# Optimization experiments

Measured on AMD Instinct MI355X. Metric: run time of the kernel, lower is better.

## Reference

```python
import jax, jax.numpy as jnp
import numpy as np

B, C, H, W = 8, 512, 32, 32


def setup_inputs() -> dict:
    key = jax.random.key(0)
    kx, kq, kk, k6 = jax.random.split(key, 4)
    std = 0.02
    return {
        "x": jax.random.normal(kx, (B, C, H, W), dtype=jnp.float32),
        "Wq": jax.random.normal(kq, (C, C), dtype=jnp.float32) * std,
        "bq": jnp.zeros((C,), dtype=jnp.float32),
        "Wk": jax.random.normal(kk, (C, C), dtype=jnp.float32) * std,
        "bk": jnp.zeros((C,), dtype=jnp.float32),
        "W6": jax.random.normal(k6, (C, C), dtype=jnp.float32) * std,
        "b6": jnp.zeros((C,), dtype=jnp.float32),
    }


def reference(x, Wq, bq, Wk, bk, W6, b6):
    b, c, h, w = x.shape
    hw = h * w
    scale = 1.0 / (c ** 0.5)
    # [B, HW, C] token-major view of the feature map
    xf = jnp.transpose(x.reshape(b, c, hw), (0, 2, 1))
    # 1x1 convs are per-pixel linear layers (weight layout: [C_out, C_in])
    q = xf @ Wq.T + bq                      # [B, HW, C]
    k = xf @ Wk.T + bk                      # [B, HW, C]
    # cross-batch attention scores: every pixel attends to every pixel of every image
    scores = q.reshape(b * hw, c) @ k.reshape(b * hw, c).T   # [B*HW, B*HW]
    s = scores.reshape(b * hw, b, hw)
    # per-query: max response within each image, then mean over images
    xw = jnp.max(s, axis=-1).mean(axis=-1)  # [B*HW]
    xw = xw.reshape(b, hw) * scale
    xw = jax.nn.softmax(xw, axis=-1).reshape(b, 1, h, w)
    x5 = x * xw                             # spatial gating
    # final 1x1 conv
    of = jnp.transpose(x5.reshape(b, c, hw), (0, 2, 1)) @ W6.T + b6
    return jnp.transpose(of, (0, 2, 1)).reshape(b, c, h, w)
```

## Files before the change

kernel.cpp:

```cpp
#include <hip/hip_runtime.h>


typedef __attribute__((ext_vector_type(8))) short bf16x8;
typedef __attribute__((ext_vector_type(4))) float f32x4;

__device__ __forceinline__ unsigned short f2bf(float f) {
  unsigned u = __builtin_bit_cast(unsigned, f);
  u += 0x7FFFu + ((u >> 16) & 1u);
  return (unsigned short)(u >> 16);
}

__device__ __forceinline__ void gload_lds16(const void* g, void* l) {
  __builtin_amdgcn_global_load_lds(
      (const __attribute__((address_space(1))) unsigned int*)g,
      (__attribute__((address_space(3))) unsigned int*)l, 16, 0, 0);
}

__global__ __launch_bounds__(256) void transpose_x(const float* __restrict__ x,
                                                   short* __restrict__ xt) {
  const int p0 = blockIdx.x * 64, c0 = blockIdx.y * 64, b = blockIdx.z;
  __shared__ float t[64][65];
  const int u = threadIdx.x;
  {
    const int p4 = u & 15, cr = u >> 4;
    for (int cc = 0; cc < 4; ++cc) {
      const int c = cc * 16 + cr;
      const float4 v = *(const float4*)&x[((size_t)(b * 512 + c0 + c)) * 1024 + p0 + p4 * 4];
      t[p4 * 4 + 0][c] = v.x;
      t[p4 * 4 + 1][c] = v.y;
      t[p4 * 4 + 2][c] = v.z;
      t[p4 * 4 + 3][c] = v.w;
    }
  }
  __syncthreads();
  {
    const int c4 = u & 15, pr = u >> 4;
    for (int pp = 0; pp < 4; ++pp) {
      const int p = pp * 16 + pr;
      ushort4 o;
      o.x = f2bf(t[p][c4 * 4 + 0]);
      o.y = f2bf(t[p][c4 * 4 + 1]);
      o.z = f2bf(t[p][c4 * 4 + 2]);
      o.w = f2bf(t[p][c4 * 4 + 3]);
      *(ushort4*)&xt[((size_t)(b * 1024 + p0 + p)) * 512 + c0 + c4 * 4] = o;
    }
  }
}

__global__ __launch_bounds__(256) void pack_w(const float* __restrict__ Wq,
                                              const float* __restrict__ Wk,
                                              const float* __restrict__ W6,
                                              short* __restrict__ wcat) {
  const int i = blockIdx.x * 256 + threadIdx.x;
  const int idx = i * 4;
  const float* src = (idx < 262144) ? Wq : (idx < 524288) ? Wk : W6;
  const float4 v = *(const float4*)&src[idx & 262143];
  ushort4 o;
  o.x = f2bf(v.x); o.y = f2bf(v.y); o.z = f2bf(v.z); o.w = f2bf(v.w);
  *(ushort4*)&wcat[idx] = o;
}

__global__ __launch_bounds__(256) void gemm_qkz(const short* __restrict__ xt,
                                                const short* __restrict__ wcat,
                                                const float* __restrict__ bq,
                                                const float* __restrict__ bk,
                                                short* __restrict__ qk,
                                                float* __restrict__ z) {
  __shared__ short lds_a[128 * 32];
  __shared__ short lds_b[128 * 32];
  const int tid = threadIdx.x;
  const int w = tid >> 6, lane = tid & 63;
  const int wr = w >> 1, wc = w & 1;
  const int quad = lane >> 4, lcol = lane & 15;
  const int srow = w * 16 + (lane >> 2);
  const int skoff = (lane & 3) * 8;
  const int m0 = blockIdx.x * 128;
  const int n0 = blockIdx.y * 128;

  f32x4 acc[4][4];
#pragma unroll
  for (int i = 0; i < 4; ++i)
#pragma unroll
    for (int j = 0; j < 4; ++j)
#pragma unroll
      for (int r = 0; r < 4; ++r) acc[i][j][r] = 0.f;

  const short* Abase = xt + (size_t)(m0 + srow) * 512 + skoff;
  const short* Bbase = wcat + (size_t)(n0 + srow) * 512 + skoff;
  short* la = lds_a + (w * 16) * 32;
  short* lb = lds_b + (w * 16) * 32;

  for (int kt = 0; kt < 16; ++kt) {
    const int kb = kt * 32;
    __syncthreads();
    gload_lds16(Abase + kb, la);
    gload_lds16(Abase + kb + (size_t)64 * 512, la + 64 * 32);
    gload_lds16(Bbase + kb, lb);
    gload_lds16(Bbase + kb + (size_t)64 * 512, lb + 64 * 32);
    __syncthreads();
    bf16x8 af[4], bf[4];
#pragma unroll
    for (int i = 0; i < 4; ++i)
      af[i] = *(const bf16x8*)&lds_a[(wr * 64 + i * 16 + lcol) * 32 + quad * 8];
#pragma unroll
    for (int j = 0; j < 4; ++j)
      bf[j] = *(const bf16x8*)&lds_b[(wc * 64 + j * 16 + lcol) * 32 + quad * 8];
#pragma unroll
    for (int i = 0; i < 4; ++i)
#pragma unroll
      for (int j = 0; j < 4; ++j)
        acc[i][j] = __builtin_amdgcn_mfma_f32_16x16x32_bf16(af[i], bf[j], acc[i][j], 0, 0, 0);
  }

  const int region = (int)blockIdx.y >> 2;
  if (region < 2) {
    const float* bias = region ? bk : bq;
#pragma unroll
    for (int i = 0; i < 4; ++i)
#pragma unroll
      for (int j = 0; j < 4; ++j) {
        const int row = m0 + wr * 64 + i * 16 + quad * 4;
        const int col = n0 + wc * 64 + j * 16 + lcol;
        const float bv = bias[col & 511];
#pragma unroll
        for (int r = 0; r < 4; ++r)
          qk[(size_t)(row + r) * 1024 + col] = (short)f2bf(acc[i][j][r] + bv);
      }
  } else {
#pragma unroll
    for (int i = 0; i < 4; ++i)
#pragma unroll
      for (int j = 0; j < 4; ++j) {
        const int row = m0 + wr * 64 + i * 16 + quad * 4;
        const int col = n0 - 1024 + wc * 64 + j * 16 + lcol;
#pragma unroll
        for (int r = 0; r < 4; ++r)
          z[(size_t)(row + r) * 512 + col] = acc[i][j][r];
      }
  }
}

__global__ __launch_bounds__(256) void gemm_scores(const short* __restrict__ qk,
                                                   float* __restrict__ wsmx) {
  __shared__ short lds_a[128 * 32];
  __shared__ short lds_b[128 * 32];
  __shared__ float partial[128][2];
  const int tid = threadIdx.x;
  const int w = tid >> 6, lane = tid & 63;
  const int wr = w >> 1, wc = w & 1;
  const int quad = lane >> 4, lcol = lane & 15;
  const int srow = w * 16 + (lane >> 2);
  const int skoff = (lane & 3) * 8;
  const int m0 = blockIdx.x * 128;
  const int n0 = blockIdx.y * 128;

  f32x4 acc[4][4];
#pragma unroll
  for (int i = 0; i < 4; ++i)
#pragma unroll
    for (int j = 0; j < 4; ++j)
#pragma unroll
      for (int r = 0; r < 4; ++r) acc[i][j][r] = 0.f;

  const short* Abase = qk + (size_t)(m0 + srow) * 1024 + skoff;
  const short* Bbase = qk + (size_t)(n0 + srow) * 1024 + 512 + skoff;
  short* la = lds_a + (w * 16) * 32;
  short* lb = lds_b + (w * 16) * 32;

  for (int kt = 0; kt < 16; ++kt) {
    const int kb = kt * 32;
    __syncthreads();
    gload_lds16(Abase + kb, la);
    gload_lds16(Abase + kb + (size_t)64 * 1024, la + 64 * 32);
    gload_lds16(Bbase + kb, lb);
    gload_lds16(Bbase + kb + (size_t)64 * 1024, lb + 64 * 32);
    __syncthreads();
    bf16x8 af[4], bf[4];
#pragma unroll
    for (int i = 0; i < 4; ++i)
      af[i] = *(const bf16x8*)&lds_a[(wr * 64 + i * 16 + lcol) * 32 + quad * 8];
#pragma unroll
    for (int j = 0; j < 4; ++j)
      bf[j] = *(const bf16x8*)&lds_b[(wc * 64 + j * 16 + lcol) * 32 + quad * 8];
#pragma unroll
    for (int i = 0; i < 4; ++i)
#pragma unroll
      for (int j = 0; j < 4; ++j)
        acc[i][j] = __builtin_amdgcn_mfma_f32_16x16x32_bf16(af[i], bf[j], acc[i][j], 0, 0, 0);
  }

#pragma unroll
  for (int i = 0; i < 4; ++i) {
#pragma unroll
    for (int r = 0; r < 4; ++r) {
      float v = fmaxf(fmaxf(acc[i][0][r], acc[i][1][r]),
                      fmaxf(acc[i][2][r], acc[i][3][r]));
#pragma unroll
      for (int off = 1; off < 16; off <<= 1) v = fmaxf(v, __shfl_xor(v, off));
      if (lcol == 0) partial[wr * 64 + i * 16 + quad * 4 + r][wc] = v;
    }
  }
  __syncthreads();
  if (tid < 128)
    wsmx[(size_t)blockIdx.y * 8192 + m0 + tid] = fmaxf(partial[tid][0], partial[tid][1]);
}

__global__ __launch_bounds__(1024) void softmax_xw(const float* __restrict__ wsmx,
                                                   float* __restrict__ xw) {
  const int b = blockIdx.x, p = threadIdx.x;
  const int m = b * 1024 + p;
  float s = 0.f;
#pragma unroll
  for (int img = 0; img < 8; ++img) {
    float mx = -1e30f;
#pragma unroll
    for (int t = 0; t < 8; ++t) mx = fmaxf(mx, wsmx[(size_t)(img * 8 + t) * 8192 + m]);
    s += mx;
  }
  const float logit = s * 0.005524271728019903f;
  __shared__ float red[16];
  float v = logit;
#pragma unroll
  for (int off = 32; off >= 1; off >>= 1) v = fmaxf(v, __shfl_xor(v, off));
  if ((p & 63) == 0) red[p >> 6] = v;
  __syncthreads();
  float bmax = red[0];
#pragma unroll
  for (int t = 1; t < 16; ++t) bmax = fmaxf(bmax, red[t]);
  const float e = expf(logit - bmax);
  float sv = e;
#pragma unroll
  for (int off = 32; off >= 1; off >>= 1) sv += __shfl_xor(sv, off);
  __syncthreads();
  if ((p & 63) == 0) red[p >> 6] = sv;
  __syncthreads();
  float bsum = 0.f;
#pragma unroll
  for (int t = 0; t < 16; ++t) bsum += red[t];
  xw[m] = e / bsum;
}

__global__ __launch_bounds__(256) void epilogue_out(const float* __restrict__ z,
                                                    const float* __restrict__ xw,
                                                    const float* __restrict__ b6,
                                                    float* __restrict__ out) {
  const int p0 = blockIdx.x * 64, c0 = blockIdx.y * 64, b = blockIdx.z;
  __shared__ float t[64][65];
  const int u = threadIdx.x;
  {
    const int c4 = u & 15, pr = u >> 4;
    for (int pp = 0; pp < 4; ++pp) {
      const int p = pp * 16 + pr;
      const float4 v = *(const float4*)&z[((size_t)(b * 1024 + p0 + p)) * 512 + c0 + c4 * 4];
      t[c4 * 4 + 0][p] = v.x;
      t[c4 * 4 + 1][p] = v.y;
      t[c4 * 4 + 2][p] = v.z;
      t[c4 * 4 + 3][p] = v.w;
    }
  }
  __syncthreads();
  {
    const int p4 = u & 15, cr = u >> 4;
    const float4 wv = *(const float4*)&xw[b * 1024 + p0 + p4 * 4];
    for (int cc = 0; cc < 4; ++cc) {
      const int co = cc * 16 + cr;
      const float bias = b6[c0 + co];
      float4 o;
      o.x = t[co][p4 * 4 + 0] * wv.x + bias;
      o.y = t[co][p4 * 4 + 1] * wv.y + bias;
      o.z = t[co][p4 * 4 + 2] * wv.z + bias;
      o.w = t[co][p4 * 4 + 3] * wv.w + bias;
      *(float4*)&out[((size_t)(b * 512 + c0 + co)) * 1024 + p0 + p4 * 4] = o;
    }
  }
}

extern "C" void kernel_launch(void* const* d_in, const int* in_sizes, int n_in,
                              void* d_out, int out_size, void* d_ws, size_t ws_size,
                              hipStream_t stream) {
  const float* x  = (const float*)d_in[0];
  const float* Wq = (const float*)d_in[1];
  const float* bq = (const float*)d_in[2];
  const float* Wk = (const float*)d_in[3];
  const float* bk = (const float*)d_in[4];
  const float* W6 = (const float*)d_in[5];
  const float* b6 = (const float*)d_in[6];
  float* out = (float*)d_out;

  char* ws = (char*)d_ws;
  short* xt   = (short*)(ws + 0);
  short* wcat = (short*)(ws + 8388608);
  short* qk   = (short*)(ws + 10485760);
  float* z    = (float*)(ws + 29360128);
  float* wsmx = (float*)(ws + 46137344);
  float* xw   = (float*)(ws + 48234496);

  transpose_x<<<dim3(16, 8, 8), 256, 0, stream>>>(x, xt);
  pack_w<<<768, 256, 0, stream>>>(Wq, Wk, W6, wcat);
  gemm_qkz<<<dim3(64, 12), 256, 0, stream>>>(xt, wcat, bq, bk, qk, z);
  gemm_scores<<<dim3(64, 64), 256, 0, stream>>>(qk, wsmx);
  softmax_xw<<<8, 1024, 0, stream>>>(wsmx, xw);
  epilogue_out<<<dim3(16, 8, 8), 256, 0, stream>>>(z, xw, b6, out);
}
```

Before: 210.9 us.

## Use FP8 scores GEMM, fuse prep kernels, and fold gating into output GEMM

Q and K are now stored as e4m3 FP8 bytes, and the 8192x8192 scores GEMM runs on fp8 MFMA instructions. This halves operand bytes and doubles the MFMA rate on the dominant stage. The transpose and weight-pack kernels are merged into one launch. The W6 projection moves out of the QK GEMM into a separate GEMM that applies the softmax gate and bias in its epilogue and writes the output directly, which removes the fp32 z buffer and the transpose epilogue. LDS layouts change to a 16-row chunk-contiguous scheme. FP8 quantization of q and k risks accuracy in the per-image max reduction.

```diff
diff --git a/kernel.cpp b/kernel.cpp
--- a/kernel.cpp
+++ b/kernel.cpp
@@ -3,6 +3,7 @@
 
 typedef __attribute__((ext_vector_type(8))) short bf16x8;
 typedef __attribute__((ext_vector_type(4))) float f32x4;
+typedef __attribute__((ext_vector_type(2))) long long i64x2;
 
 __device__ __forceinline__ unsigned short f2bf(float f) {
   unsigned u = __builtin_bit_cast(unsigned, f);
@@ -10,72 +11,82 @@
   return (unsigned short)(u >> 16);
 }
 
+__device__ __forceinline__ unsigned char f2e4m3(float x) {
+  unsigned u = __builtin_bit_cast(unsigned, x);
+  unsigned char s = (unsigned char)((u >> 24) & 0x80u);
+  unsigned a = u & 0x7FFFFFFFu;
+  if (a >= 0x43E00000u) return s | 0x7Eu;
+  if (a < 0x3C800000u) {
+    float q = __builtin_bit_cast(float, a) * 512.f;
+    int m = (int)(q + 0.5f);
+    return s | (unsigned char)m;
+  }
+  unsigned r = a + 0x7FFFFu + ((a >> 20) & 1u);
+  int e = (int)((r >> 23) & 0xFF) - 127;
+  if (e > 8) return s | 0x7Eu;
+  unsigned m3 = (r >> 20) & 0x7u;
+  return s | (unsigned char)(((e + 7) << 3) | m3);
+}
+
 __device__ __forceinline__ void gload_lds16(const void* g, void* l) {
   __builtin_amdgcn_global_load_lds(
       (const __attribute__((address_space(1))) unsigned int*)g,
       (__attribute__((address_space(3))) unsigned int*)l, 16, 0, 0);
 }
 
-__global__ __launch_bounds__(256) void transpose_x(const float* __restrict__ x,
-                                                   short* __restrict__ xt) {
-  const int p0 = blockIdx.x * 64, c0 = blockIdx.y * 64, b = blockIdx.z;
-  __shared__ float t[64][65];
-  const int u = threadIdx.x;
-  {
-    const int p4 = u & 15, cr = u >> 4;
-    for (int cc = 0; cc < 4; ++cc) {
-      const int c = cc * 16 + cr;
-      const float4 v = *(const float4*)&x[((size_t)(b * 512 + c0 + c)) * 1024 + p0 + p4 * 4];
-      t[p4 * 4 + 0][c] = v.x;
-      t[p4 * 4 + 1][c] = v.y;
-      t[p4 * 4 + 2][c] = v.z;
-      t[p4 * 4 + 3][c] = v.w;
-    }
-  }
-  __syncthreads();
-  {
-    const int c4 = u & 15, pr = u >> 4;
-    for (int pp = 0; pp < 4; ++pp) {
-      const int p = pp * 16 + pr;
-      ushort4 o;
-      o.x = f2bf(t[p][c4 * 4 + 0]);
-      o.y = f2bf(t[p][c4 * 4 + 1]);
-      o.z = f2bf(t[p][c4 * 4 + 2]);
-      o.w = f2bf(t[p][c4 * 4 + 3]);
-      *(ushort4*)&xt[((size_t)(b * 1024 + p0 + p)) * 512 + c0 + c4 * 4] = o;
-    }
-  }
-}
-
-__global__ __launch_bounds__(256) void pack_w(const float* __restrict__ Wq,
-                                              const float* __restrict__ Wk,
-                                              const float* __restrict__ W6,
-                                              short* __restrict__ wcat) {
-  const int i = blockIdx.x * 256 + threadIdx.x;
-  const int idx = i * 4;
-  const float* src = (idx < 262144) ? Wq : (idx < 524288) ? Wk : W6;
-  const float4 v = *(const float4*)&src[idx & 262143];
-  ushort4 o;
-  o.x = f2bf(v.x); o.y = f2bf(v.y); o.z = f2bf(v.z); o.w = f2bf(v.w);
-  *(ushort4*)&wcat[idx] = o;
-}
-
-__global__ __launch_bounds__(256) void gemm_qkz(const short* __restrict__ xt,
-                                                const short* __restrict__ wcat,
-                                                const float* __restrict__ bq,
-                                                const float* __restrict__ bk,
-                                                short* __restrict__ qk,
-                                                float* __restrict__ z) {
+__global__ __launch_bounds__(256) void prep(const float* __restrict__ x,
+                                            const float* __restrict__ Wq,
+                                            const float* __restrict__ Wk,
+                                            const float* __restrict__ W6,
+                                            short* __restrict__ xt,
+                                            short* __restrict__ wcat) {
+  const int bid = blockIdx.x, u = threadIdx.x;
+  if (bid < 1024) {
+    const int p0 = (bid & 15) * 64, c0 = ((bid >> 4) & 7) * 64, b = bid >> 7;
+    __shared__ float t[64][65];
+    {
+      const int p4 = u & 15, cr = u >> 4;
+      for (int cc = 0; cc < 4; ++cc) {
+        const int c = cc * 16 + cr;
+        const float4 v = *(const float4*)&x[((size_t)(b * 512 + c0 + c)) * 1024 + p0 + p4 * 4];
+        t[p4 * 4 + 0][c] = v.x; t[p4 * 4 + 1][c] = v.y;
+        t[p4 * 4 + 2][c] = v.z; t[p4 * 4 + 3][c] = v.w;
+      }
+    }
+    __syncthreads();
+    {
+      const int c4 = u & 15, pr = u >> 4;
+      for (int pp = 0; pp < 4; ++pp) {
+        const int p = pp * 16 + pr;
+        ushort4 o;
+        o.x = f2bf(t[p][c4 * 4 + 0]); o.y = f2bf(t[p][c4 * 4 + 1]);
+        o.z = f2bf(t[p][c4 * 4 + 2]); o.w = f2bf(t[p][c4 * 4 + 3]);
+        *(ushort4*)&xt[((size_t)(b * 1024 + p0 + p)) * 512 + c0 + c4 * 4] = o;
+      }
+    }
+  } else {
+    const int i = (bid - 1024) * 256 + u;
+    const int idx = i * 4;
+    const float* src = (idx < 262144) ? Wq : (idx < 524288) ? Wk : W6;
+    const float4 v = *(const float4*)&src[idx & 262143];
+    ushort4 o;
+    o.x = f2bf(v.x); o.y = f2bf(v.y); o.z = f2bf(v.z); o.w = f2bf(v.w);
+    *(ushort4*)&wcat[idx] = o;
+  }
+}
+
+__global__ __launch_bounds__(256) void gemm_qk(const short* __restrict__ xt,
+                                               const short* __restrict__ wcat,
+                                               const float* __restrict__ bq,
+                                               const float* __restrict__ bk,
+                                               unsigned char* __restrict__ qk8) {
   __shared__ short lds_a[128 * 32];
   __shared__ short lds_b[128 * 32];
-  const int tid = threadIdx.x;
-  const int w = tid >> 6, lane = tid & 63;
+  const int tid = threadIdx.x, w = tid >> 6, lane = tid & 63;
   const int wr = w >> 1, wc = w & 1;
   const int quad = lane >> 4, lcol = lane & 15;
-  const int srow = w * 16 + (lane >> 2);
-  const int skoff = (lane & 3) * 8;
-  const int m0 = blockIdx.x * 128;
-  const int n0 = blockIdx.y * 128;
+  const int skq = lane >> 4, srow = lane & 15;
+  const int m0 = blockIdx.x * 128, n0 = blockIdx.y * 128;
 
   f32x4 acc[4][4];
 #pragma unroll
@@ -85,26 +96,22 @@
 #pragma unroll
       for (int r = 0; r < 4; ++r) acc[i][j][r] = 0.f;
 
-  const short* Abase = xt + (size_t)(m0 + srow) * 512 + skoff;
-  const short* Bbase = wcat + (size_t)(n0 + srow) * 512 + skoff;
-  short* la = lds_a + (w * 16) * 32;
-  short* lb = lds_b + (w * 16) * 32;
+  const short* Abase = xt + (size_t)(m0 + srow) * 512 + skq * 8;
+  const short* Bbase = wcat + (size_t)(n0 + srow) * 512 + skq * 8;
 
   for (int kt = 0; kt < 16; ++kt) {
     const int kb = kt * 32;
     __syncthreads();
-    gload_lds16(Abase + kb, la);
-    gload_lds16(Abase + kb + (size_t)64 * 512, la + 64 * 32);
-    gload_lds16(Bbase + kb, lb);
-    gload_lds16(Bbase + kb + (size_t)64 * 512, lb + 64 * 32);
+    gload_lds16(Abase + (size_t)(w * 16) * 512 + kb,       lds_a + w * 512);
+    gload_lds16(Abase + (size_t)((4 + w) * 16) * 512 + kb, lds_a + (4 + w) * 512);
+    gload_lds16(Bbase + (size_t)(w * 16) * 512 + kb,       lds_b + w * 512);
+    gload_lds16(Bbase + (size_t)((4 + w) * 16) * 512 + kb, lds_b + (4 + w) * 512);
     __syncthreads();
     bf16x8 af[4], bf[4];
 #pragma unroll
-    for (int i = 0; i < 4; ++i)
-      af[i] = *(const bf16x8*)&lds_a[(wr * 64 + i * 16 + lcol) * 32 + quad * 8];
-#pragma unroll
-    for (int j = 0; j < 4; ++j)
-      bf[j] = *(const bf16x8*)&lds_b[(wc * 64 + j * 16 + lcol) * 32 + quad * 8];
+    for (int i = 0; i < 4; ++i) af[i] = *(const bf16x8*)&lds_a[(wr * 4 + i) * 512 + lane * 8];
+#pragma unroll
+    for (int j = 0; j < 4; ++j) bf[j] = *(const bf16x8*)&lds_b[(wc * 4 + j) * 512 + lane * 8];
 #pragma unroll
     for (int i = 0; i < 4; ++i)
 #pragma unroll
@@ -112,47 +119,30 @@
         acc[i][j] = __builtin_amdgcn_mfma_f32_16x16x32_bf16(af[i], bf[j], acc[i][j], 0, 0, 0);
   }
 
-  const int region = (int)blockIdx.y >> 2;
-  if (region < 2) {
-    const float* bias = region ? bk : bq;
-#pragma unroll
-    for (int i = 0; i < 4; ++i)
-#pragma unroll
-      for (int j = 0; j < 4; ++j) {
-        const int row = m0 + wr * 64 + i * 16 + quad * 4;
-        const int col = n0 + wc * 64 + j * 16 + lcol;
-        const float bv = bias[col & 511];
-#pragma unroll
-        for (int r = 0; r < 4; ++r)
-          qk[(size_t)(row + r) * 1024 + col] = (short)f2bf(acc[i][j][r] + bv);
-      }
-  } else {
-#pragma unroll
-    for (int i = 0; i < 4; ++i)
-#pragma unroll
-      for (int j = 0; j < 4; ++j) {
-        const int row = m0 + wr * 64 + i * 16 + quad * 4;
-        const int col = n0 - 1024 + wc * 64 + j * 16 + lcol;
-#pragma unroll
-        for (int r = 0; r < 4; ++r)
-          z[(size_t)(row + r) * 512 + col] = acc[i][j][r];
-      }
-  }
-}
-
-__global__ __launch_bounds__(256) void gemm_scores(const short* __restrict__ qk,
+  const float* bias = (blockIdx.y >= 4) ? bk : bq;
+#pragma unroll
+  for (int i = 0; i < 4; ++i)
+#pragma unroll
+    for (int j = 0; j < 4; ++j) {
+      const int row = m0 + wr * 64 + i * 16 + quad * 4;
+      const int col = n0 + wc * 64 + j * 16 + lcol;
+      const float bv = bias[col & 511];
+#pragma unroll
+      for (int r = 0; r < 4; ++r)
+        qk8[(size_t)(row + r) * 1024 + col] = f2e4m3(acc[i][j][r] + bv);
+    }
+}
+
+__global__ __launch_bounds__(256) void gemm_scores(const unsigned char* __restrict__ qk8,
                                                    float* __restrict__ wsmx) {
-  __shared__ short lds_a[128 * 32];
-  __shared__ short lds_b[128 * 32];
+  __shared__ unsigned char lds_a[8192];
+  __shared__ unsigned char lds_b[8192];
   __shared__ float partial[128][2];
-  const int tid = threadIdx.x;
-  const int w = tid >> 6, lane = tid & 63;
+  const int tid = threadIdx.x, w = tid >> 6, lane = tid & 63;
   const int wr = w >> 1, wc = w & 1;
   const int quad = lane >> 4, lcol = lane & 15;
-  const int srow = w * 16 + (lane >> 2);
-  const int skoff = (lane & 3) * 8;
-  const int m0 = blockIdx.x * 128;
-  const int n0 = blockIdx.y * 128;
+  const int skq = lane >> 4, srow = lane & 15;
+  const int m0 = blockIdx.x * 128, n0 = blockIdx.y * 128;
 
   f32x4 acc[4][4];
 #pragma unroll
@@ -162,31 +152,29 @@
 #pragma unroll
       for (int r = 0; r < 4; ++r) acc[i][j][r] = 0.f;
 
-  const short* Abase = qk + (size_t)(m0 + srow) * 1024 + skoff;
-  const short* Bbase = qk + (size_t)(n0 + srow) * 1024 + 512 + skoff;
-  short* la = lds_a + (w * 16) * 32;
-  short* lb = lds_b + (w * 16) * 32;
-
-  for (int kt = 0; kt < 16; ++kt) {
-    const int kb = kt * 32;
-    __syncthreads();
-    gload_lds16(Abase + kb, la);
-    gload_lds16(Abase + kb + (size_t)64 * 1024, la + 64 * 32);
-    gload_lds16(Bbase + kb, lb);
-    gload_lds16(Bbase + kb + (size_t)64 * 1024, lb + 64 * 32);
-    __syncthreads();
-    bf16x8 af[4], bf[4];
+  const unsigned char* Abase = qk8 + (size_t)(m0 + srow) * 1024 + skq * 16;
+  const unsigned char* Bbase = qk8 + (size_t)(n0 + srow) * 1024 + 512 + skq * 16;
+
+  for (int kt = 0; kt < 8; ++kt) {
+    const int kb = kt * 64;
+    __syncthreads();
+    gload_lds16(Abase + (size_t)(w * 16) * 1024 + kb,       lds_a + w * 1024);
+    gload_lds16(Abase + (size_t)((4 + w) * 16) * 1024 + kb, lds_a + (4 + w) * 1024);
+    gload_lds16(Bbase + (size_t)(w * 16) * 1024 + kb,       lds_b + w * 1024);
+    gload_lds16(Bbase + (size_t)((4 + w) * 16) * 1024 + kb, lds_b + (4 + w) * 1024);
+    __syncthreads();
+    i64x2 af[4], bf[4];
+#pragma unroll
+    for (int i = 0; i < 4; ++i) af[i] = *(const i64x2*)&lds_a[(wr * 4 + i) * 1024 + lane * 16];
+#pragma unroll
+    for (int j = 0; j < 4; ++j) bf[j] = *(const i64x2*)&lds_b[(wc * 4 + j) * 1024 + lane * 16];
 #pragma unroll
     for (int i = 0; i < 4; ++i)
-      af[i] = *(const bf16x8*)&lds_a[(wr * 64 + i * 16 + lcol) * 32 + quad * 8];
-#pragma unroll
-    for (int j = 0; j < 4; ++j)
-      bf[j] = *(const bf16x8*)&lds_b[(wc * 64 + j * 16 + lcol) * 32 + quad * 8];
-#pragma unroll
-    for (int i = 0; i < 4; ++i)
-#pragma unroll
-      for (int j = 0; j < 4; ++j)
-        acc[i][j] = __builtin_amdgcn_mfma_f32_16x16x32_bf16(af[i], bf[j], acc[i][j], 0, 0, 0);
+#pragma unroll
+      for (int j = 0; j < 4; ++j) {
+        acc[i][j] = __builtin_amdgcn_mfma_f32_16x16x32_fp8_fp8(af[i].x, bf[j].x, acc[i][j], 0, 0, 0);
+        acc[i][j] = __builtin_amdgcn_mfma_f32_16x16x32_fp8_fp8(af[i].y, bf[j].y, acc[i][j], 0, 0, 0);
+      }
   }
 
 #pragma unroll
@@ -240,37 +228,65 @@
   xw[m] = e / bsum;
 }
 
-__global__ __launch_bounds__(256) void epilogue_out(const float* __restrict__ z,
-                                                    const float* __restrict__ xw,
-                                                    const float* __restrict__ b6,
-                                                    float* __restrict__ out) {
-  const int p0 = blockIdx.x * 64, c0 = blockIdx.y * 64, b = blockIdx.z;
-  __shared__ float t[64][65];
-  const int u = threadIdx.x;
-  {
-    const int c4 = u & 15, pr = u >> 4;
-    for (int pp = 0; pp < 4; ++pp) {
-      const int p = pp * 16 + pr;
-      const float4 v = *(const float4*)&z[((size_t)(b * 1024 + p0 + p)) * 512 + c0 + c4 * 4];
-      t[c4 * 4 + 0][p] = v.x;
-      t[c4 * 4 + 1][p] = v.y;
-      t[c4 * 4 + 2][p] = v.z;
-      t[c4 * 4 + 3][p] = v.w;
-    }
-  }
-  __syncthreads();
-  {
-    const int p4 = u & 15, cr = u >> 4;
-    const float4 wv = *(const float4*)&xw[b * 1024 + p0 + p4 * 4];
-    for (int cc = 0; cc < 4; ++cc) {
-      const int co = cc * 16 + cr;
-      const float bias = b6[c0 + co];
+__global__ __launch_bounds__(256) void gemm_out(const short* __restrict__ xt,
+                                                const short* __restrict__ wcat,
+                                                const float* __restrict__ xw,
+                                                const float* __restrict__ b6,
+                                                float* __restrict__ out) {
+  __shared__ short lds_a[128 * 32];
+  __shared__ short lds_b[128 * 32];
+  const int tid = threadIdx.x, w = tid >> 6, lane = tid & 63;
+  const int wr = w >> 1, wc = w & 1;
+  const int quad = lane >> 4, lcol = lane & 15;
+  const int skq = lane >> 4, srow = lane & 15;
+  const int m0 = blockIdx.x * 128, n0 = blockIdx.y * 128;
+
+  f32x4 acc[4][4];
+#pragma unroll
+  for (int i = 0; i < 4; ++i)
+#pragma unroll
+    for (int j = 0; j < 4; ++j)
+#pragma unroll
+      for (int r = 0; r < 4; ++r) acc[i][j][r] = 0.f;
+
+  const short* Abase = xt + (size_t)(m0 + srow) * 512 + skq * 8;
+  const short* Bbase = wcat + (size_t)(1024 + n0 + srow) * 512 + skq * 8;
+
+  for (int kt = 0; kt < 16; ++kt) {
+    const int kb = kt * 32;
+    __syncthreads();
+    gload_lds16(Abase + (size_t)(w * 16) * 512 + kb,       lds_a + w * 512);
+    gload_lds16(Abase + (size_t)((4 + w) * 16) * 512 + kb, lds_a + (4 + w) * 512);
+    gload_lds16(Bbase + (size_t)(w * 16) * 512 + kb,       lds_b + w * 512);
+    gload_lds16(Bbase + (size_t)((4 + w) * 16) * 512 + kb, lds_b + (4 + w) * 512);
+    __syncthreads();
+    bf16x8 af[4], bf[4];
+#pragma unroll
+    for (int i = 0; i < 4; ++i) af[i] = *(const bf16x8*)&lds_a[(wr * 4 + i) * 512 + lane * 8];
+#pragma unroll
+    for (int j = 0; j < 4; ++j) bf[j] = *(const bf16x8*)&lds_b[(wc * 4 + j) * 512 + lane * 8];
+#pragma unroll
+    for (int i = 0; i < 4; ++i)
+#pragma unroll
+      for (int j = 0; j < 4; ++j)
+        acc[i][j] = __builtin_amdgcn_mfma_f32_16x16x32_bf16(af[i], bf[j], acc[i][j], 0, 0, 0);
+  }
+
+#pragma unroll
+  for (int i = 0; i < 4; ++i) {
+    const int mbase = m0 + wr * 64 + i * 16 + quad * 4;
+    const int b = mbase >> 10, p = mbase & 1023;
+    const float4 wv = *(const float4*)&xw[mbase];
+#pragma unroll
+    for (int j = 0; j < 4; ++j) {
+      const int col = n0 + wc * 64 + j * 16 + lcol;
+      const float bias = b6[col];
       float4 o;
-      o.x = t[co][p4 * 4 + 0] * wv.x + bias;
-      o.y = t[co][p4 * 4 + 1] * wv.y + bias;
-      o.z = t[co][p4 * 4 + 2] * wv.z + bias;
-      o.w = t[co][p4 * 4 + 3] * wv.w + bias;
-      *(float4*)&out[((size_t)(b * 512 + c0 + co)) * 1024 + p0 + p4 * 4] = o;
+      o.x = acc[i][j][0] * wv.x + bias;
+      o.y = acc[i][j][1] * wv.y + bias;
+      o.z = acc[i][j][2] * wv.z + bias;
+      o.w = acc[i][j][3] * wv.w + bias;
+      *(float4*)&out[((size_t)(b * 512 + col)) * 1024 + p] = o;
     }
   }
 }
@@ -288,17 +304,15 @@
   float* out = (float*)d_out;
 
   char* ws = (char*)d_ws;
-  short* xt   = (short*)(ws + 0);
-  short* wcat = (short*)(ws + 8388608);
-  short* qk   = (short*)(ws + 10485760);
-  float* z    = (float*)(ws + 29360128);
-  float* wsmx = (float*)(ws + 46137344);
-  float* xw   = (float*)(ws + 48234496);
-
-  transpose_x<<<dim3(16, 8, 8), 256, 0, stream>>>(x, xt);
-  pack_w<<<768, 256, 0, stream>>>(Wq, Wk, W6, wcat);
-  gemm_qkz<<<dim3(64, 12), 256, 0, stream>>>(xt, wcat, bq, bk, qk, z);
-  gemm_scores<<<dim3(64, 64), 256, 0, stream>>>(qk, wsmx);
+  short* xt          = (short*)(ws + 0);
+  short* wcat        = (short*)(ws + 8388608);
+  unsigned char* qk8 = (unsigned char*)(ws + 10485760);
+  float* wsmx        = (float*)(ws + 18874368);
+  float* xw          = (float*)(ws + 20971520);
+
+  prep<<<1792, 256, 0, stream>>>(x, Wq, Wk, W6, xt, wcat);
+  gemm_qk<<<dim3(64, 8), 256, 0, stream>>>(xt, wcat, bq, bk, qk8);
+  gemm_scores<<<dim3(64, 64), 256, 0, stream>>>(qk8, wsmx);
   softmax_xw<<<8, 1024, 0, stream>>>(wsmx, xw);
-  epilogue_out<<<dim3(16, 8, 8), 256, 0, stream>>>(z, xw, b6, out);
-}
+  gemm_out<<<dim3(64, 4), 256, 0, stream>>>(xt, wcat, xw, b6, out);
+}
```

Result: faster. 195.0 us (-7.6%).
